# Kernel tuning notes

Measured on AMD Instinct MI355X. Metric: run time of the kernel, lower is better.

## Reference

```python
import jax, jax.numpy as jnp
import numpy as np

G = 32        # group_num
PD = 8        # primary capsule dim
OC = 10       # output caps (classes)
OD = 16       # output dim
GS = 36       # group_size = primary spatial 6*6
N_ITERS = 3   # routing iterations


def conv2d(x, w, stride):
    return jax.lax.conv_general_dilated(
        x, w, window_strides=(stride, stride), padding='VALID',
        dimension_numbers=('NCHW', 'OIHW', 'NCHW'))


def squash(x):
    l2 = jnp.sum(x * x, axis=-1, keepdims=True)
    l = jnp.sqrt(l2)
    return x * (l2 / (1.0 + l2)) / (l + 1e-8)


def setup_inputs() -> dict:
    key = jax.random.key(0)
    ks = jax.random.split(key, 6)
    B = 256
    inp = jax.random.normal(ks[0], (B, 1, 28, 28), dtype=jnp.float32)
    W1 = jax.random.normal(ks[1], (256, 1, 9, 9), dtype=jnp.float32) * 0.05
    b1 = jnp.zeros((256,), dtype=jnp.float32)
    W2 = jax.random.normal(ks[2], (G * PD, 256, 9, 9), dtype=jnp.float32) * 0.01
    b2 = jnp.zeros((G * PD,), dtype=jnp.float32)
    Wcaps = jax.random.normal(ks[3], (G, GS, PD, OC * OD), dtype=jnp.float32) * 0.01
    b_route = jnp.zeros((G, 1, GS, OC), dtype=jnp.float32)
    return {'input': inp, 'W1': W1, 'b1': b1, 'W2': W2, 'b2': b2,
            'Wcaps': Wcaps, 'b_route': b_route}


def reference(input, W1, b1, W2, b2, Wcaps, b_route):
    B = input.shape[0]
    # conv1 + relu: (B,256,20,20)
    x = jax.nn.relu(conv2d(input, W1, 1) + b1[None, :, None, None])
    # primary caps conv: (B,256,6,6)
    y = conv2d(x, W2, 2) + b2[None, :, None, None]
    H = y.shape[2]
    # (B,G,PD,H,W) -> (B,G,H,W,PD) -> (B,G,GS,PD)
    y = y.reshape(B, G, PD, H, H).transpose(0, 1, 3, 4, 2).reshape(B, G, GS, PD)
    u = squash(y)
    # capsule predictions: (B,G,GS,OC,OD)
    up = jnp.einsum('bgsi,gsio->bgso', u, Wcaps).reshape(B, G, GS, OC, OD)
    # routing logits: (B,G,GS,OC)
    b = jnp.broadcast_to(jnp.transpose(b_route, (1, 0, 2, 3)), (B, G, GS, OC))
    v = None
    for r in range(N_ITERS):
        c = jax.nn.softmax(b, axis=3)                       # (B,G,GS,OC)
        s = jnp.einsum('bgso,bgsod->bgod', c, up)           # (B,G,OC,OD)
        v = squash(s)
        if r < N_ITERS - 1:
            b = b + jnp.einsum('bgsod,bgod->bgso', up, v)
    v = v.sum(axis=1)                                       # (B,OC,OD)
    probs = jnp.sqrt(jnp.sum(v * v, axis=2))                # (B,OC)
    return v, probs
```

## Files before the change

kernel.cpp:

```cpp
#include <hip/hip_runtime.h>
#include <math.h>


typedef float floatx4 __attribute__((ext_vector_type(4)));
typedef __bf16 bf16x8 __attribute__((ext_vector_type(8)));
typedef unsigned uintx4 __attribute__((ext_vector_type(4)));

#define XHI_OFF 0u
#define XLO_OFF 58720256u
#define WHI_OFF 117440512u
#define WLO_OFF 128974848u
#define Y2_OFF  140509184u
#define VP_OFF  0u
#define Y2_BYTES 9437184u
#define Y2_FLOATS 2359296

#define SL_IY   88
#define SL_IMG  1760
#define SL_PAR  7072
#define SL_STRIDE 14336

#define TAPSTRIDE 65536

__device__ __forceinline__ void bf16split(float v, short& hs, short& ls) {
  unsigned u = __builtin_bit_cast(unsigned, v);
  unsigned r = (u + 0x7FFFu + ((u >> 16) & 1u)) & 0xFFFF0000u;
  hs = (short)(r >> 16);
  float lo = v - __builtin_bit_cast(float, r);
  unsigned u2 = __builtin_bit_cast(unsigned, lo);
  unsigned r2 = u2 + 0x7FFFu + ((u2 >> 16) & 1u);
  ls = (short)(r2 >> 16);
}

__device__ __forceinline__ void stage7(const short* gp, short* lp) {
#pragma unroll
  for (int c = 0; c < 7; c++)
    __builtin_amdgcn_global_load_lds(
        (const __attribute__((address_space(1))) void*)(gp + c * 512),
        (__attribute__((address_space(3))) void*)(lp + c * 512), 16, 0, 0);
}

__global__ __launch_bounds__(320) void conv1_k(
    const float* __restrict__ inp, const float* __restrict__ W1,
    const float* __restrict__ b1, short* __restrict__ xhi,
    short* __restrict__ xlo) {
  __shared__ __align__(16) float img[784];
  __shared__ float wl[81 * 34];
  const int blk = blockIdx.x;
  const int b = blk >> 3;
  const int cbase = (blk & 7) * 32;
  const int t = threadIdx.x;

  const float4* src = (const float4*)(inp + b * 784);
  for (int idx = t; idx < 196; idx += 320) ((float4*)img)[idx] = src[idx];
  for (int idx = t; idx < 2592; idx += 320) {
    int c = idx / 81, tap = idx - c * 81;
    wl[tap * 34 + c] = W1[(cbase + c) * 81 + tap];
  }
  __syncthreads();

  const int oy = t >> 4;
  const int ct = t & 15;
  const int c0 = cbase + ct * 2;
  const float bias0 = b1[c0], bias1 = b1[c0 + 1];
  float acc0[20], acc1[20];
#pragma unroll
  for (int ox = 0; ox < 20; ox++) { acc0[ox] = bias0; acc1[ox] = bias1; }

#pragma unroll 1
  for (int i = 0; i < 9; i++) {
    float wr0[9], wr1[9];
#pragma unroll
    for (int j = 0; j < 9; j++) {
      float2 wv = *(const float2*)&wl[(i * 9 + j) * 34 + ct * 2];
      wr0[j] = wv.x; wr1[j] = wv.y;
    }
    float xr[28];
    const float4* rp = (const float4*)&img[(oy + i) * 28];
#pragma unroll
    for (int k = 0; k < 7; k++) {
      float4 v = rp[k];
      xr[4 * k] = v.x; xr[4 * k + 1] = v.y; xr[4 * k + 2] = v.z; xr[4 * k + 3] = v.w;
    }
#pragma unroll
    for (int j = 0; j < 9; j++)
#pragma unroll
      for (int ox = 0; ox < 20; ox++) {
        acc0[ox] = fmaf(xr[ox + j], wr0[j], acc0[ox]);
        acc1[ox] = fmaf(xr[ox + j], wr1[j], acc1[ox]);
      }
  }

  const int icgG = c0 >> 3;
  const long sbase = ((long)(icgG * 64 + (b >> 2))) * SL_STRIDE
                   + (long)(b & 3) * SL_IMG + (long)oy * SL_IY + (c0 & 7);
#pragma unroll
  for (int ox = 0; ox < 20; ox++) {
    float v0 = fmaxf(acc0[ox], 0.f), v1 = fmaxf(acc1[ox], 0.f);
    short h0, l0, h1, l1;
    bf16split(v0, h0, l0);
    bf16split(v1, h1, l1);
    long a = sbase + (ox & 1) * SL_PAR + (ox >> 1) * 8;
    *(short2*)&xhi[a] = make_short2(h0, h1);
    *(short2*)&xlo[a] = make_short2(l0, l1);
  }
  {
    long a0 = sbase + 80;
    *(short2*)&xhi[a0] = make_short2(0, 0);
    *(short2*)&xlo[a0] = make_short2(0, 0);
    long a1 = sbase + SL_PAR + 80;
    *(short2*)&xhi[a1] = make_short2(0, 0);
    *(short2*)&xlo[a1] = make_short2(0, 0);
  }
}

__global__ __launch_bounds__(256) void wtrans_k(
    const float* __restrict__ W2, short* __restrict__ whi,
    short* __restrict__ wlo) {
  __shared__ short lh[81 * 258];
  __shared__ short ll[81 * 258];
  const int blk = blockIdx.x;
  const int icg = blk & 31, ocg = blk >> 5;
  const int t = threadIdx.x;

  for (int idx = t; idx < 20736; idx += 256) {
    int c = idx / 648, r = idx - c * 648;
    int ics = r / 81, tap = r - ics * 81;
    float v = W2[(long)(ocg * 32 + c) * 20736 + icg * 648 + r];
    short h, l;
    bf16split(v, h, l);
    lh[tap * 258 + c * 8 + ics] = h;
    ll[tap * 258 + c * 8 + ics] = l;
  }
  __syncthreads();
  const long obase = (long)icg * 2048 + ocg * 256 + t;
#pragma unroll 1
  for (int tap = 0; tap < 88; tap++) {
    short h = 0, l = 0;
    if (tap < 81) { h = lh[tap * 258 + t]; l = ll[tap * 258 + t]; }
    whi[obase + (long)tap * TAPSTRIDE] = h;
    wlo[obase + (long)tap * TAPSTRIDE] = l;
  }
}

template <bool SPLIT>
__global__ __launch_bounds__(256, 2) void conv2_k(
    const short* __restrict__ xhi, const short* __restrict__ xlo,
    const short* __restrict__ whi, const short* __restrict__ wlo,
    float* __restrict__ y2) {
  __shared__ __align__(16) short slab[2][SL_STRIDE];

  const int blk = blockIdx.x;
  const int ks = blk & 7;
  const int mb = blk >> 3;
  const int t = threadIdx.x;
  const int lane = t & 63;
  const int q = lane >> 4;
  const int ln16 = lane & 15;
  const int wv = t >> 6;

  int combo[9];
#pragma unroll
  for (int mt = 0; mt < 9; mt++) {
    int row = mt * 16 + ln16;
    int im = row / 36;
    int pos = row - im * 36;
    int oy = pos / 6, ox = pos - oy * 6;
    combo[mt] = im * SL_IMG + oy * (2 * SL_IY) + ox * 8;
  }

  floatx4 acc[9][4];
#pragma unroll
  for (int mt = 0; mt < 9; mt++)
#pragma unroll
    for (int nt = 0; nt < 4; nt++) acc[mt][nt] = (floatx4)0.f;

  const int stoff = wv * 7 * 512 + lane * 8;

  stage7(xhi + (long)(ks * 4 * 64 + mb) * SL_STRIDE + stoff, &slab[0][stoff]);

#pragma unroll 1
  for (int icg = 0; icg < 4; icg++) {
    const int icgG = ks * 4 + icg;
    const long wb0 = ((long)icgG * 256 + wv * 64 + ln16) * 8 + (long)q * TAPSTRIDE;

    __syncthreads();
    stage7(xlo + (long)(icgG * 64 + mb) * SL_STRIDE + stoff, &slab[1][stoff]);

    {
      bf16x8 cbh[4], cbl[4];
#pragma unroll
      for (int nt = 0; nt < 4; nt++) {
        cbh[nt] = *(const bf16x8*)&whi[wb0 + nt * 128];
        cbl[nt] = *(const bf16x8*)&wlo[wb0 + nt * 128];
      }
      int ip = 0, jp = q;
      int aoff = (jp & 1) * SL_PAR + (jp >> 1) * 8;
      bf16x8 a0 = *(const bf16x8*)&slab[0][aoff + combo[0]];
      bf16x8 a1 = *(const bf16x8*)&slab[0][aoff + combo[1]];
      bf16x8 a2 = *(const bf16x8*)&slab[0][aoff + combo[2]];
#pragma unroll 1
      for (int kst = 0; kst < 21; kst++) {
        const int t0n = (kst < 20) ? (kst + 1) * 4 : 80;
        bf16x8 nbh[4], nbl[4];
#pragma unroll
        for (int nt = 0; nt < 4; nt++) {
          nbh[nt] = *(const bf16x8*)&whi[wb0 + (long)t0n * TAPSTRIDE + nt * 128];
          nbl[nt] = *(const bf16x8*)&wlo[wb0 + (long)t0n * TAPSTRIDE + nt * 128];
        }
        int jn = jp + 4, in_ = ip;
        if (jn >= 9) { jn -= 9; in_++; }
        const int aoff_n = (jn & 1) * SL_PAR + in_ * SL_IY + (jn >> 1) * 8;
#pragma unroll
        for (int bb = 0; bb < 3; bb++) {
          const int poff = (bb < 2) ? aoff : aoff_n;
          const int cb = (bb < 2) ? (bb + 1) * 3 : 0;
          bf16x8 n0 = *(const bf16x8*)&slab[0][poff + combo[cb + 0]];
          bf16x8 n1 = *(const bf16x8*)&slab[0][poff + combo[cb + 1]];
          bf16x8 n2 = *(const bf16x8*)&slab[0][poff + combo[cb + 2]];
#pragma unroll
          for (int nt = 0; nt < 4; nt++) {
            acc[bb * 3 + 0][nt] = __builtin_amdgcn_mfma_f32_16x16x32_bf16(
                a0, cbh[nt], acc[bb * 3 + 0][nt], 0, 0, 0);
            acc[bb * 3 + 1][nt] = __builtin_amdgcn_mfma_f32_16x16x32_bf16(
                a1, cbh[nt], acc[bb * 3 + 1][nt], 0, 0, 0);
            acc[bb * 3 + 2][nt] = __builtin_amdgcn_mfma_f32_16x16x32_bf16(
                a2, cbh[nt], acc[bb * 3 + 2][nt], 0, 0, 0);
          }
#pragma unroll
          for (int nt = 0; nt < 4; nt++) {
            acc[bb * 3 + 0][nt] = __builtin_amdgcn_mfma_f32_16x16x32_bf16(
                a0, cbl[nt], acc[bb * 3 + 0][nt], 0, 0, 0);
            acc[bb * 3 + 1][nt] = __builtin_amdgcn_mfma_f32_16x16x32_bf16(
                a1, cbl[nt], acc[bb * 3 + 1][nt], 0, 0, 0);
            acc[bb * 3 + 2][nt] = __builtin_amdgcn_mfma_f32_16x16x32_bf16(
                a2, cbl[nt], acc[bb * 3 + 2][nt], 0, 0, 0);
          }
          a0 = n0; a1 = n1; a2 = n2;
        }
#pragma unroll
        for (int nt = 0; nt < 4; nt++) { cbh[nt] = nbh[nt]; cbl[nt] = nbl[nt]; }
        aoff = aoff_n; ip = in_; jp = jn;
      }
    }

    __syncthreads();
    if (icg < 3)
      stage7(xhi + (long)((icgG + 1) * 64 + mb) * SL_STRIDE + stoff, &slab[0][stoff]);

    {
      bf16x8 cbh[4];
#pragma unroll
      for (int nt = 0; nt < 4; nt++) cbh[nt] = *(const bf16x8*)&whi[wb0 + nt * 128];
      int ip = 0, jp = q;
      int aoff = (jp & 1) * SL_PAR + (jp >> 1) * 8;
      bf16x8 a0 = *(const bf16x8*)&slab[1][aoff + combo[0]];
      bf16x8 a1 = *(const bf16x8*)&slab[1][aoff + combo[1]];
      bf16x8 a2 = *(const bf16x8*)&slab[1][aoff + combo[2]];
#pragma unroll 1
      for (int kst = 0; kst < 21; kst++) {
        const int t0n = (kst < 20) ? (kst + 1) * 4 : 80;
        bf16x8 nbh[4];
#pragma unroll
        for (int nt = 0; nt < 4; nt++)
          nbh[nt] = *(const bf16x8*)&whi[wb0 + (long)t0n * TAPSTRIDE + nt * 128];
        int jn = jp + 4, in_ = ip;
        if (jn >= 9) { jn -= 9; in_++; }
        const int aoff_n = (jn & 1) * SL_PAR + in_ * SL_IY + (jn >> 1) * 8;
#pragma unroll
        for (int bb = 0; bb < 3; bb++) {
          const int poff = (bb < 2) ? aoff : aoff_n;
          const int cb = (bb < 2) ? (bb + 1) * 3 : 0;
          bf16x8 n0 = *(const bf16x8*)&slab[1][poff + combo[cb + 0]];
          bf16x8 n1 = *(const bf16x8*)&slab[1][poff + combo[cb + 1]];
          bf16x8 n2 = *(const bf16x8*)&slab[1][poff + combo[cb + 2]];
#pragma unroll
          for (int nt = 0; nt < 4; nt++) {
            acc[bb * 3 + 0][nt] = __builtin_amdgcn_mfma_f32_16x16x32_bf16(
                a0, cbh[nt], acc[bb * 3 + 0][nt], 0, 0, 0);
            acc[bb * 3 + 1][nt] = __builtin_amdgcn_mfma_f32_16x16x32_bf16(
                a1, cbh[nt], acc[bb * 3 + 1][nt], 0, 0, 0);
            acc[bb * 3 + 2][nt] = __builtin_amdgcn_mfma_f32_16x16x32_bf16(
                a2, cbh[nt], acc[bb * 3 + 2][nt], 0, 0, 0);
          }
          a0 = n0; a1 = n1; a2 = n2;
        }
#pragma unroll
        for (int nt = 0; nt < 4; nt++) cbh[nt] = nbh[nt];
        aoff = aoff_n; ip = in_; jp = jn;
      }
    }
  }

  {
    float* dst = y2 + (SPLIT ? (long)ks * Y2_FLOATS : 0l);
#pragma unroll
    for (int mt = 0; mt < 9; mt++)
#pragma unroll
      for (int nt = 0; nt < 4; nt++) {
        const int oc = wv * 64 + nt * 16 + ln16;
        const int gg = oc >> 3, dd = oc & 7;
#pragma unroll
        for (int r = 0; r < 4; r++) {
          const int lr = mt * 16 + q * 4 + r;
          const int im = lr / 36;
          const int s = lr - im * 36;
          const long a = ((long)(gg * 256 + mb * 4 + im) * 36 + s) * 8 + dd;
          if (SPLIT) dst[a] = acc[mt][nt][r];
          else       atomicAdd(&dst[a], acc[mt][nt][r]);
        }
      }
  }
}

template <bool SPLIT>
__global__ __launch_bounds__(256) void caps_k(
    const float* __restrict__ y2, const float* __restrict__ b2,
    const float* __restrict__ Wcaps, const float* __restrict__ b_route,
    float* __restrict__ vpart) {
  __shared__ float u[288];
  __shared__ float usc[36];
  __shared__ __align__(16) float up[5760];
  __shared__ float bl[360];
  __shared__ float cl[360];
  __shared__ float sv[160];
  __shared__ float vv[160];
  __shared__ float scale[10];
  const int blk = blockIdx.x;
  const int g = blk & 31, b = blk >> 5;
  const int t = threadIdx.x;

  {
    const long base = ((long)g * 256 + b) * 288;
    for (int idx = t; idx < 288; idx += 256) {
      float a;
      if (SPLIT) {
        a = 0.f;
#pragma unroll
        for (int ks = 0; ks < 8; ks++) a += y2[(long)ks * Y2_FLOATS + base + idx];
      } else {
        a = y2[base + idx];
      }
      u[idx] = a + b2[g * 8 + (idx & 7)];
    }
  }
  for (int idx = t; idx < 360; idx += 256) bl[idx] = b_route[g * 360 + idx];
  __syncthreads();
  if (t < 36) {
    float l2 = 0.f;
#pragma unroll
    for (int d = 0; d < 8; d++) { float v = u[t * 8 + d]; l2 = fmaf(v, v, l2); }
    float l = sqrtf(l2);
    usc[t] = (l2 / (1.f + l2)) / (l + 1e-8f);
  }
  __syncthreads();
  for (int idx = t; idx < 288; idx += 256) u[idx] *= usc[idx >> 3];
  __syncthreads();
  for (int idx = t; idx < 1440; idx += 256) {
    int s = idx / 40, k4 = idx - s * 40;
    const float4* wp4 = (const float4*)(Wcaps + (long)(g * 36 + s) * 1280) + k4;
    float4 a = make_float4(0.f, 0.f, 0.f, 0.f);
#pragma unroll
    for (int d = 0; d < 8; d++) {
      float uv = u[s * 8 + d];
      float4 w = wp4[d * 40];
      a.x = fmaf(uv, w.x, a.x); a.y = fmaf(uv, w.y, a.y);
      a.z = fmaf(uv, w.z, a.z); a.w = fmaf(uv, w.w, a.w);
    }
    ((float4*)up)[idx] = a;
  }
  __syncthreads();

  for (int r = 0; r < 3; r++) {
    if (t < 36) {
      float m = bl[t * 10];
#pragma unroll
      for (int oc = 1; oc < 10; oc++) m = fmaxf(m, bl[t * 10 + oc]);
      float e[10]; float sum = 0.f;
#pragma unroll
      for (int oc = 0; oc < 10; oc++) { e[oc] = expf(bl[t * 10 + oc] - m); sum += e[oc]; }
      float inv = 1.f / sum;
#pragma unroll
      for (int oc = 0; oc < 10; oc++) cl[t * 10 + oc] = e[oc] * inv;
    }
    __syncthreads();
    if (t < 160) {
      const int oc = t >> 4;
      float a = 0.f;
#pragma unroll 1
      for (int s = 0; s < 36; s++) a = fmaf(cl[s * 10 + oc], up[s * 160 + t], a);
      sv[t] = a;
    }
    __syncthreads();
    if (t < 10) {
      float l2 = 0.f;
#pragma unroll
      for (int od = 0; od < 16; od++) { float v = sv[t * 16 + od]; l2 = fmaf(v, v, l2); }
      scale[t] = (l2 / (1.f + l2)) / (sqrtf(l2) + 1e-8f);
    }
    __syncthreads();
    if (t < 160) vv[t] = sv[t] * scale[t >> 4];
    __syncthreads();
    if (r < 2) {
      for (int idx = t; idx < 360; idx += 256) {
        int s = idx / 10, oc = idx - s * 10;
        float a = 0.f;
#pragma unroll
        for (int od = 0; od < 16; od++)
          a = fmaf(up[s * 160 + oc * 16 + od], vv[oc * 16 + od], a);
        bl[idx] += a;
      }
      __syncthreads();
    }
  }
  if (t < 160) vpart[(b * 32 + g) * 160 + t] = vv[t];
}

__global__ __launch_bounds__(192) void final_k(
    const float* __restrict__ vpart, float* __restrict__ out) {
  __shared__ float v[160];
  const int b = blockIdx.x, t = threadIdx.x;
  if (t < 160) {
    float a = 0.f;
#pragma unroll 4
    for (int g = 0; g < 32; g++) a += vpart[(b * 32 + g) * 160 + t];
    v[t] = a;
    out[b * 160 + t] = a;
  }
  __syncthreads();
  if (t < 10) {
    float l2 = 0.f;
#pragma unroll
    for (int od = 0; od < 16; od++) { float x = v[t * 16 + od]; l2 = fmaf(x, x, l2); }
    out[40960 + b * 10 + t] = sqrtf(l2);
  }
}

extern "C" void kernel_launch(void* const* d_in, const int* in_sizes, int n_in,
                              void* d_out, int out_size, void* d_ws, size_t ws_size,
                              hipStream_t stream) {
  const float* inp     = (const float*)d_in[0];
  const float* W1      = (const float*)d_in[1];
  const float* b1      = (const float*)d_in[2];
  const float* W2      = (const float*)d_in[3];
  const float* b2      = (const float*)d_in[4];
  const float* Wcaps   = (const float*)d_in[5];
  const float* b_route = (const float*)d_in[6];
  float* out = (float*)d_out;
  char* ws = (char*)d_ws;

  short* xhi = (short*)(ws + XHI_OFF);
  short* xlo = (short*)(ws + XLO_OFF);
  short* whi = (short*)(ws + WHI_OFF);
  short* wlo = (short*)(ws + WLO_OFF);
  float* y2  = (float*)(ws + Y2_OFF);
  float* vp  = (float*)(ws + VP_OFF);

  const bool split = ws_size >= (size_t)Y2_OFF + 8ull * Y2_BYTES;

  conv1_k <<<2048, 320, 0, stream>>>(inp, W1, b1, xhi, xlo);
  wtrans_k<<<256, 256, 0, stream>>>(W2, whi, wlo);
  if (split) {
    conv2_k<true> <<<512, 256, 0, stream>>>(xhi, xlo, whi, wlo, y2);
    caps_k<true>  <<<8192, 256, 0, stream>>>(y2, b2, Wcaps, b_route, vp);
  } else {
    (void)hipMemsetAsync(y2, 0, Y2_BYTES, stream);
    conv2_k<false> <<<512, 256, 0, stream>>>(xhi, xlo, whi, wlo, y2);
    caps_k<false>  <<<8192, 256, 0, stream>>>(y2, b2, Wcaps, b_route, vp);
  }
  final_k <<<256, 192, 0, stream>>>(vp, out);
}
```

Measured before the change: 486.0 us.

## Fuse conv1 and weight transform into one launch; process two images per caps block

Merges the conv1 kernel and the W2 bf16-split transpose kernel into a single launch, with the first 256 blocks doing the weight transform in four tap chunks so shared memory fits the conv1 footprint. The capsule routing kernel now handles two batch images per block, so each Wcaps load is reused for both images and the grid is halved. This removes one launch and halves Wcaps traffic, at the cost of doubled shared memory per caps block, which may lower occupancy, and more barriers in the chunked weight transform.

Measured after the change: 518.1 us. 1.07x slower.

```diff
diff --git a/kernel.cpp b/kernel.cpp
--- a/kernel.cpp
+++ b/kernel.cpp
@@ -40,16 +40,64 @@
         (__attribute__((address_space(3))) void*)(lp + c * 512), 16, 0, 0);
 }
 
-__global__ __launch_bounds__(320) void conv1_k(
+__global__ __launch_bounds__(320) void pre_k(
     const float* __restrict__ inp, const float* __restrict__ W1,
-    const float* __restrict__ b1, short* __restrict__ xhi,
-    short* __restrict__ xlo) {
-  __shared__ __align__(16) float img[784];
-  __shared__ float wl[81 * 34];
-  const int blk = blockIdx.x;
+    const float* __restrict__ b1, const float* __restrict__ W2,
+    short* __restrict__ xhi, short* __restrict__ xlo,
+    short* __restrict__ whi, short* __restrict__ wlo) {
+  __shared__ __align__(16) char smem[21672];
+  const int t = threadIdx.x;
+
+  if (blockIdx.x < 256) {
+    short* lh = (short*)smem;
+    short* ll = (short*)(smem + 10836);
+    const int blk = blockIdx.x;
+    const int icg = blk & 31, ocg = blk >> 5;
+    const long obase = (long)icg * 2048 + ocg * 256 + t;
+
+#pragma unroll 1
+    for (int p = 0; p < 4; p++) {
+      for (int idx = t; idx < 5376; idx += 320) {
+        int c = idx / 168, r = idx - c * 168;
+        int ics = r / 21, tapl = r - ics * 21;
+        int tap = p * 21 + tapl;
+        if (tap < 81) {
+          float v = W2[(long)(ocg * 32 + c) * 20736 + icg * 648 + ics * 81 + tap];
+          short h, l;
+          bf16split(v, h, l);
+          lh[tapl * 258 + c * 8 + ics] = h;
+          ll[tapl * 258 + c * 8 + ics] = l;
+        }
+      }
+      __syncthreads();
+      if (t < 256) {
+#pragma unroll 1
+        for (int tapl = 0; tapl < 21; tapl++) {
+          int tap = p * 21 + tapl;
+          if (tap >= 84) break;
+          short h = 0, l = 0;
+          if (tap < 81) { h = lh[tapl * 258 + t]; l = ll[tapl * 258 + t]; }
+          whi[obase + (long)tap * TAPSTRIDE] = h;
+          wlo[obase + (long)tap * TAPSTRIDE] = l;
+        }
+      }
+      __syncthreads();
+    }
+    if (t < 256) {
+#pragma unroll
+      for (int tap = 84; tap < 88; tap++) {
+        whi[obase + (long)tap * TAPSTRIDE] = 0;
+        wlo[obase + (long)tap * TAPSTRIDE] = 0;
+      }
+    }
+    return;
+  }
+
+  float* img = (float*)smem;
+  float* wl  = (float*)(smem + 3136);
+  const int blk = blockIdx.x - 256;
   const int b = blk >> 3;
   const int cbase = (blk & 7) * 32;
-  const int t = threadIdx.x;
 
   const float4* src = (const float4*)(inp + b * 784);
   for (int idx = t; idx < 196; idx += 320) ((float4*)img)[idx] = src[idx];
@@ -111,35 +159,6 @@
     long a1 = sbase + SL_PAR + 80;
     *(short2*)&xhi[a1] = make_short2(0, 0);
     *(short2*)&xlo[a1] = make_short2(0, 0);
-  }
-}
-
-__global__ __launch_bounds__(256) void wtrans_k(
-    const float* __restrict__ W2, short* __restrict__ whi,
-    short* __restrict__ wlo) {
-  __shared__ short lh[81 * 258];
-  __shared__ short ll[81 * 258];
-  const int blk = blockIdx.x;
-  const int icg = blk & 31, ocg = blk >> 5;
-  const int t = threadIdx.x;
-
-  for (int idx = t; idx < 20736; idx += 256) {
-    int c = idx / 648, r = idx - c * 648;
-    int ics = r / 81, tap = r - ics * 81;
-    float v = W2[(long)(ocg * 32 + c) * 20736 + icg * 648 + r];
-    short h, l;
-    bf16split(v, h, l);
-    lh[tap * 258 + c * 8 + ics] = h;
-    ll[tap * 258 + c * 8 + ics] = l;
-  }
-  __syncthreads();
-  const long obase = (long)icg * 2048 + ocg * 256 + t;
-#pragma unroll 1
-  for (int tap = 0; tap < 88; tap++) {
-    short h = 0, l = 0;
-    if (tap < 81) { h = lh[tap * 258 + t]; l = ll[tap * 258 + t]; }
-    whi[obase + (long)tap * TAPSTRIDE] = h;
-    wlo[obase + (long)tap * TAPSTRIDE] = l;
   }
 }
 
@@ -318,21 +337,21 @@
     const float* __restrict__ y2, const float* __restrict__ b2,
     const float* __restrict__ Wcaps, const float* __restrict__ b_route,
     float* __restrict__ vpart) {
-  __shared__ float u[288];
-  __shared__ float usc[36];
-  __shared__ __align__(16) float up[5760];
-  __shared__ float bl[360];
-  __shared__ float cl[360];
-  __shared__ float sv[160];
-  __shared__ float vv[160];
-  __shared__ float scale[10];
+  __shared__ float u[2][288];
+  __shared__ float usc[2][36];
+  __shared__ __align__(16) float up[2][5760];
+  __shared__ float bl[2][360];
+  __shared__ float cl[2][360];
+  __shared__ float sv[2][160];
+  __shared__ float vv[2][160];
+  __shared__ float scale[2][10];
   const int blk = blockIdx.x;
-  const int g = blk & 31, b = blk >> 5;
+  const int g = blk & 31, bp = blk >> 5;
   const int t = threadIdx.x;
 
   {
-    const long base = ((long)g * 256 + b) * 288;
-    for (int idx = t; idx < 288; idx += 256) {
+    const long base = ((long)g * 256 + 2 * bp) * 288;
+    for (int idx = t; idx < 576; idx += 256) {
       float a;
       if (SPLIT) {
         a = 0.f;
@@ -341,79 +360,100 @@
       } else {
         a = y2[base + idx];
       }
-      u[idx] = a + b2[g * 8 + (idx & 7)];
-    }
-  }
-  for (int idx = t; idx < 360; idx += 256) bl[idx] = b_route[g * 360 + idx];
+      const int im = idx >= 288;
+      u[im][idx - im * 288] = a + b2[g * 8 + (idx & 7)];
+    }
+  }
+  for (int idx = t; idx < 720; idx += 256) {
+    const int im = idx >= 360;
+    bl[im][idx - im * 360] = b_route[g * 360 + (idx - im * 360)];
+  }
   __syncthreads();
-  if (t < 36) {
+  if (t < 72) {
+    const int im = t >= 36, s = t - im * 36;
     float l2 = 0.f;
 #pragma unroll
-    for (int d = 0; d < 8; d++) { float v = u[t * 8 + d]; l2 = fmaf(v, v, l2); }
+    for (int d = 0; d < 8; d++) { float v = u[im][s * 8 + d]; l2 = fmaf(v, v, l2); }
     float l = sqrtf(l2);
-    usc[t] = (l2 / (1.f + l2)) / (l + 1e-8f);
+    usc[im][s] = (l2 / (1.f + l2)) / (l + 1e-8f);
   }
   __syncthreads();
-  for (int idx = t; idx < 288; idx += 256) u[idx] *= usc[idx >> 3];
+  for (int idx = t; idx < 576; idx += 256) {
+    const int im = idx >= 288, i = idx - im * 288;
+    u[im][i] *= usc[im][i >> 3];
+  }
   __syncthreads();
   for (int idx = t; idx < 1440; idx += 256) {
     int s = idx / 40, k4 = idx - s * 40;
     const float4* wp4 = (const float4*)(Wcaps + (long)(g * 36 + s) * 1280) + k4;
-    float4 a = make_float4(0.f, 0.f, 0.f, 0.f);
+    float4 a0 = make_float4(0.f, 0.f, 0.f, 0.f);
+    float4 a1 = make_float4(0.f, 0.f, 0.f, 0.f);
 #pragma unroll
     for (int d = 0; d < 8; d++) {
-      float uv = u[s * 8 + d];
       float4 w = wp4[d * 40];
-      a.x = fmaf(uv, w.x, a.x); a.y = fmaf(uv, w.y, a.y);
-      a.z = fmaf(uv, w.z, a.z); a.w = fmaf(uv, w.w, a.w);
-    }
-    ((float4*)up)[idx] = a;
+      float u0 = u[0][s * 8 + d], u1 = u[1][s * 8 + d];
+      a0.x = fmaf(u0, w.x, a0.x); a0.y = fmaf(u0, w.y, a0.y);
+      a0.z = fmaf(u0, w.z, a0.z); a0.w = fmaf(u0, w.w, a0.w);
+      a1.x = fmaf(u1, w.x, a1.x); a1.y = fmaf(u1, w.y, a1.y);
+      a1.z = fmaf(u1, w.z, a1.z); a1.w = fmaf(u1, w.w, a1.w);
+    }
+    ((float4*)up[0])[idx] = a0;
+    ((float4*)up[1])[idx] = a1;
   }
   __syncthreads();
 
   for (int r = 0; r < 3; r++) {
-    if (t < 36) {
-      float m = bl[t * 10];
-#pragma unroll
-      for (int oc = 1; oc < 10; oc++) m = fmaxf(m, bl[t * 10 + oc]);
+    if (t < 72) {
+      const int im = t >= 36, s = t - im * 36;
+      float m = bl[im][s * 10];
+#pragma unroll
+      for (int oc = 1; oc < 10; oc++) m = fmaxf(m, bl[im][s * 10 + oc]);
       float e[10]; float sum = 0.f;
 #pragma unroll
-      for (int oc = 0; oc < 10; oc++) { e[oc] = expf(bl[t * 10 + oc] - m); sum += e[oc]; }
+      for (int oc = 0; oc < 10; oc++) { e[oc] = expf(bl[im][s * 10 + oc] - m); sum += e[oc]; }
       float inv = 1.f / sum;
 #pragma unroll
-      for (int oc = 0; oc < 10; oc++) cl[t * 10 + oc] = e[oc] * inv;
+      for (int oc = 0; oc < 10; oc++) cl[im][s * 10 + oc] = e[oc] * inv;
     }
     __syncthreads();
     if (t < 160) {
       const int oc = t >> 4;
-      float a = 0.f;
-#pragma unroll 1
-      for (int s = 0; s < 36; s++) a = fmaf(cl[s * 10 + oc], up[s * 160 + t], a);
-      sv[t] = a;
+#pragma unroll
+      for (int im = 0; im < 2; im++) {
+        float a = 0.f;
+#pragma unroll 1
+        for (int s = 0; s < 36; s++) a = fmaf(cl[im][s * 10 + oc], up[im][s * 160 + t], a);
+        sv[im][t] = a;
+      }
     }
     __syncthreads();
-    if (t < 10) {
+    if (t < 20) {
+      const int im = t >= 10, oc = t - im * 10;
       float l2 = 0.f;
 #pragma unroll
-      for (int od = 0; od < 16; od++) { float v = sv[t * 16 + od]; l2 = fmaf(v, v, l2); }
-      scale[t] = (l2 / (1.f + l2)) / (sqrtf(l2) + 1e-8f);
+      for (int od = 0; od < 16; od++) { float v = sv[im][oc * 16 + od]; l2 = fmaf(v, v, l2); }
+      scale[im][oc] = (l2 / (1.f + l2)) / (sqrtf(l2) + 1e-8f);
     }
     __syncthreads();
-    if (t < 160) vv[t] = sv[t] * scale[t >> 4];
+    if (t < 160) { vv[0][t] = sv[0][t] * scale[0][t >> 4]; vv[1][t] = sv[1][t] * scale[1][t >> 4]; }
     __syncthreads();
     if (r < 2) {
-      for (int idx = t; idx < 360; idx += 256) {
-        int s = idx / 10, oc = idx - s * 10;
+      for (int idx = t; idx < 720; idx += 256) {
+        const int im = idx >= 360, i = idx - im * 360;
+        int s = i / 10, oc = i - s * 10;
         float a = 0.f;
 #pragma unroll
         for (int od = 0; od < 16; od++)
-          a = fmaf(up[s * 160 + oc * 16 + od], vv[oc * 16 + od], a);
-        bl[idx] += a;
+          a = fmaf(up[im][s * 160 + oc * 16 + od], vv[im][oc * 16 + od], a);
+        bl[im][i] += a;
       }
       __syncthreads();
     }
   }
-  if (t < 160) vpart[(b * 32 + g) * 160 + t] = vv[t];
+  if (t < 160) {
+    vpart[((2 * bp) * 32 + g) * 160 + t] = vv[0][t];
+    vpart[((2 * bp + 1) * 32 + g) * 160 + t] = vv[1][t];
+  }
 }
 
 __global__ __launch_bounds__(192) void final_k(
@@ -458,15 +498,14 @@
 
   const bool split = ws_size >= (size_t)Y2_OFF + 8ull * Y2_BYTES;
 
-  conv1_k <<<2048, 320, 0, stream>>>(inp, W1, b1, xhi, xlo);
-  wtrans_k<<<256, 256, 0, stream>>>(W2, whi, wlo);
+  pre_k <<<2304, 320, 0, stream>>>(inp, W1, b1, W2, xhi, xlo, whi, wlo);
   if (split) {
     conv2_k<true> <<<512, 256, 0, stream>>>(xhi, xlo, whi, wlo, y2);
-    caps_k<true>  <<<8192, 256, 0, stream>>>(y2, b2, Wcaps, b_route, vp);
+    caps_k<true>  <<<4096, 256, 0, stream>>>(y2, b2, Wcaps, b_route, vp);
   } else {
     (void)hipMemsetAsync(y2, 0, Y2_BYTES, stream);
     conv2_k<false> <<<512, 256, 0, stream>>>(xhi, xlo, whi, wlo, y2);
-    caps_k<false>  <<<8192, 256, 0, stream>>>(y2, b2, Wcaps, b_route, vp);
+    caps_k<false>  <<<4096, 256, 0, stream>>>(y2, b2, Wcaps, b_route, vp);
   }
   final_k <<<256, 192, 0, stream>>>(vp, out);
 }
```
